# Optimization experiments

Measured on AMD Instinct MI355X. Metric: run time of the kernel, lower is better.

The kernel has to match this reference:

```python
import jax, jax.numpy as jnp
import numpy as np

B, C, W, H = 8, 256, 64, 64
DQK = C // 8  # 32


def setup_inputs() -> dict:
    key = jax.random.key(0)
    ks = jax.random.split(key, 5)
    x = jax.random.normal(ks[0], (B, C, W, H), dtype=jnp.float32)
    # 1x1 conv weights as [out_ch, in_ch]; scaled ~ spectral-normalized magnitude
    w_q = jax.random.normal(ks[1], (DQK, C), dtype=jnp.float32) * (1.0 / np.sqrt(C))
    w_k = jax.random.normal(ks[2], (DQK, C), dtype=jnp.float32) * (1.0 / np.sqrt(C))
    w_v = jax.random.normal(ks[3], (C, C), dtype=jnp.float32) * (1.0 / np.sqrt(C))
    b_q = jnp.zeros((DQK,), dtype=jnp.float32)
    b_k = jnp.zeros((DQK,), dtype=jnp.float32)
    b_v = jnp.zeros((C,), dtype=jnp.float32)
    gamma = jax.random.normal(ks[4], (1,), dtype=jnp.float32)
    return {"x": x, "w_q": w_q, "b_q": b_q, "w_k": w_k, "b_k": b_k,
            "w_v": w_v, "b_v": b_v, "gamma": gamma}


def reference(x, w_q, b_q, w_k, b_k, w_v, b_v, gamma):
    b, c, w, h = x.shape
    n = w * h
    xf = x.reshape(b, c, n)  # [B, C, N]
    # 1x1 convs == channel-mixing matmuls
    q = jnp.einsum('dc,bcn->bnd', w_q, xf) + b_q  # [B, N, Dqk]
    k = jnp.einsum('dc,bcn->bdn', w_k, xf) + b_k[None, :, None]  # [B, Dqk, N]
    v = jnp.einsum('oc,bcn->bon', w_v, xf) + b_v[None, :, None]  # [B, C, N]
    energy = jnp.einsum('bnd,bdm->bnm', q, k)  # [B, N, N]
    attn = jax.nn.softmax(energy, axis=-1)
    # out[b,c,i] = sum_j v[b,c,j] * attn[b,i,j]  (bmm(v, attn^T))
    out = jnp.einsum('bcj,bij->bci', v, attn).reshape(b, c, w, h)
    return gamma[0] * out + x
```

## Files before the change

### kernel.cpp

```cpp
#include <hip/hip_runtime.h>
#include <hip/hip_bf16.h>

typedef __attribute__((ext_vector_type(8))) short short8;
typedef __attribute__((ext_vector_type(4))) float f32x4;
typedef __attribute__((ext_vector_type(16))) float f32x16;

#define NB 8
#define NC 256
#define NN 4096
#define ND 32
#define NCH 16
#define LOG2E 1.44269504088896340736f

#define PIDX(row, col) (((row) << 8) + ((col) ^ (((row) & 15) << 3)))

static __device__ __forceinline__ ushort f2bf(float f) {
  __hip_bfloat16 h = __float2bfloat16(f);
  return reinterpret_cast<ushort&>(h);
}
static __device__ __forceinline__ float bf2f(ushort u) {
  const uint v = ((uint)u) << 16;
  return __builtin_bit_cast(float, v);
}

#define LDW 264
#define LDX 40
#define LDO 136

__global__ __launch_bounds__(256, 2)
void proj_kernel(const float* __restrict__ x,
                 const float* __restrict__ wq, const float* __restrict__ bq,
                 const float* __restrict__ wk, const float* __restrict__ bk,
                 const float* __restrict__ wv, const float* __restrict__ bv,
                 ushort* __restrict__ qk, ushort* __restrict__ vt) {
  __shared__ __align__(16) ushort Ws[2][64 * LDW];
  __shared__ __align__(16) ushort Xs[128 * LDX];

  const int n0 = blockIdx.x * 128;
  const int o0 = blockIdx.y * 64;
  const int b  = blockIdx.z;
  const int t  = threadIdx.x;
  const int w  = t >> 6;
  const int lane = t & 63;
  const int g16  = lane >> 4;
  const int c16  = lane & 15;

  {
    const int o  = t >> 2;
    const int cb = (t & 3) * 64;
    const int oa = o0 + o;
    const float* wrow;
    float scale = 1.0f;
    if (oa < 32)       { wrow = wq + (size_t)oa * NC; scale = LOG2E; }
    else if (oa < 64)  { wrow = wk + (size_t)(oa - 32) * NC; }
    else               { wrow = wv + (size_t)(oa - 64) * NC; }
#pragma unroll
    for (int cc = 0; cc < 64; cc += 8) {
      const float4 f0 = *(const float4*)(wrow + cb + cc);
      const float4 f1 = *(const float4*)(wrow + cb + cc + 4);
      float v[8] = {f0.x, f0.y, f0.z, f0.w, f1.x, f1.y, f1.z, f1.w};
      union { ushort u[8]; uint4 q; } hi, lo;
#pragma unroll
      for (int e = 0; e < 8; ++e) {
        const float s = v[e] * scale;
        const ushort h = f2bf(s);
        hi.u[e] = h;
        lo.u[e] = f2bf(s - bf2f(h));
      }
      *(uint4*)&Ws[0][o * LDW + cb + cc] = hi.q;
      *(uint4*)&Ws[1][o * LDW + cb + cc] = lo.q;
    }
  }

  f32x4 acc[8];
#pragma unroll
  for (int nt = 0; nt < 8; ++nt)
#pragma unroll
    for (int r = 0; r < 4; ++r) acc[nt][r] = 0.f;

  const int s_cc = w * 8 + (lane >> 3);
  const int s_nb = (lane & 7) * 4;

  for (int c0 = 0; c0 < NC; c0 += 32) {
    __syncthreads();
    {
      const float* xsrc = x + ((size_t)(b * NC + c0 + s_cc)) * NN + n0 + s_nb;
#pragma unroll
      for (int it = 0; it < 4; ++it) {
        const float4 f = *(const float4*)(xsrc + it * 32);
        const int n = s_nb + it * 32;
        Xs[(n + 0) * LDX + s_cc] = f2bf(f.x);
        Xs[(n + 1) * LDX + s_cc] = f2bf(f.y);
        Xs[(n + 2) * LDX + s_cc] = f2bf(f.z);
        Xs[(n + 3) * LDX + s_cc] = f2bf(f.w);
      }
    }
    __syncthreads();

    const short8 ah = *(const short8*)&Ws[0][(w * 16 + c16) * LDW + c0 + g16 * 8];
    const short8 al = *(const short8*)&Ws[1][(w * 16 + c16) * LDW + c0 + g16 * 8];
#pragma unroll
    for (int nt = 0; nt < 8; ++nt) {
      const short8 bf = *(const short8*)&Xs[(nt * 16 + c16) * LDX + g16 * 8];
      acc[nt] = __builtin_amdgcn_mfma_f32_16x16x32_bf16(ah, bf, acc[nt], 0, 0, 0);
      acc[nt] = __builtin_amdgcn_mfma_f32_16x16x32_bf16(al, bf, acc[nt], 0, 0, 0);
    }
  }

  if (blockIdx.y == 0) {
    float bb[4];
#pragma unroll
    for (int r = 0; r < 4; ++r) {
      const int o = w * 16 + g16 * 4 + r;
      bb[r] = (o < 32) ? bq[o] * LOG2E : bk[o - 32];
    }
#pragma unroll
    for (int nt = 0; nt < 8; ++nt) {
      union { ushort u[4]; uint2 v; } pk;
#pragma unroll
      for (int r = 0; r < 4; ++r) pk.u[r] = f2bf(acc[nt][r] + bb[r]);
      const int n = n0 + nt * 16 + c16;
      *(uint2*)(qk + ((size_t)(b * NN + n)) * 64 + w * 16 + g16 * 4) = pk.v;
    }
  } else {
    const int ch0 = o0 - 64;
    float bb[4];
#pragma unroll
    for (int r = 0; r < 4; ++r) bb[r] = bv[ch0 + w * 16 + g16 * 4 + r];
    __syncthreads();
    ushort* Os = &Ws[0][0];
#pragma unroll
    for (int nt = 0; nt < 8; ++nt) {
#pragma unroll
      for (int r = 0; r < 4; ++r)
        Os[(w * 16 + g16 * 4 + r) * LDO + nt * 16 + c16] =
            f2bf(acc[nt][r] + bb[r]);
    }
    __syncthreads();
    const int chl = t >> 2;
    const int nb  = (t & 3) * 32;
    ushort* dst = vt + ((size_t)(b * NC + ch0 + chl)) * NN + n0 + nb;
#pragma unroll
    for (int k = 0; k < 4; ++k)
      *(uint4*)(dst + k * 8) = *(const uint4*)&Os[chl * LDO + nb + k * 8];
  }
}

__global__ __launch_bounds__(512, 1)
void attn_kernel(const ushort* __restrict__ qk, const ushort* __restrict__ vt,
                 const float* __restrict__ x, const float* __restrict__ gamma,
                 float* __restrict__ out) {
  __shared__ __align__(16) ushort P[2][128 * 256];
  __shared__ __align__(16) float lL[128];

  const int lin  = blockIdx.x;
  const int b    = lin & 7;
  const int i0   = (lin >> 3) * 128;
  const int t    = threadIdx.x;
  const int w    = t >> 6;
  const int lane = t & 63;
  const int g16  = lane >> 4;
  const int c16  = lane & 15;
  const int l5   = lane >> 5;
  const int c32  = lane & 31;

  const f32x4 zero = {0.f, 0.f, 0.f, 0.f};
  const bool isS = (w < 4);

  const int prow0 = w * 32 + c16;
  const int prow1 = prow0 + 16;
  short8 qf0, qf1;
  short8 kf[8];
  float lp0 = 0.f, lp1 = 0.f;
  const ushort* kbase = qk + ((size_t)b * NN) * 64 + 32 + g16 * 8;
  if (isS) {
    qf0 = *(const short8*)(qk + ((size_t)(b * NN + i0 + prow0)) * 64 + g16 * 8);
    qf1 = *(const short8*)(qk + ((size_t)(b * NN + i0 + prow1)) * 64 + g16 * 8);
  }

  const int p = w - 4;
  f32x16 OA[4], OB[4];
  const ushort* vbA = nullptr; const ushort* vbB = nullptr;
  if (!isS) {
#pragma unroll
    for (int isub = 0; isub < 4; ++isub)
#pragma unroll
      for (int e = 0; e < 16; ++e) { OA[isub][e] = 0.f; OB[isub][e] = 0.f; }
    vbA = vt + ((size_t)(b * NC + p * 64 + c32)) * NN + l5 * 8;
    vbB = vt + ((size_t)(b * NC + p * 64 + 32 + c32)) * NN + l5 * 8;
  }

  for (int iv = 0; iv <= NCH; ++iv) {
    if (isS) {
      if (iv < NCH) {
        ushort* Pb = P[iv & 1];
        const ushort* kch = kbase + (size_t)iv * 256 * 64;
#pragma unroll
        for (int h = 0; h < 2; ++h) {
#pragma unroll
          for (int jt = 0; jt < 8; ++jt)
            kf[jt] = *(const short8*)(
                kch + (size_t)(h * 128 + jt * 16 + c16) * 64);
#pragma unroll
          for (int jt = 0; jt < 8; ++jt) {
            const f32x4 s0 = __builtin_amdgcn_mfma_f32_16x16x32_bf16(
                kf[jt], qf0, zero, 0, 0, 0);
            const f32x4 s1 = __builtin_amdgcn_mfma_f32_16x16x32_bf16(
                kf[jt], qf1, zero, 0, 0, 0);
            union { ushort u[4]; uint2 v; } pk0, pk1;
#pragma unroll
            for (int r = 0; r < 4; ++r) {
              const float e0 = exp2f(s0[r]);
              const float e1 = exp2f(s1[r]);
              lp0 += e0; lp1 += e1;
              pk0.u[r] = f2bf(e0); pk1.u[r] = f2bf(e1);
            }
            const int col = h * 128 + jt * 16 + g16 * 4;
            *(uint2*)&Pb[PIDX(prow0, col)] = pk0.v;
            *(uint2*)&Pb[PIDX(prow1, col)] = pk1.v;
          }
        }
      } else {
        lp0 += __shfl_xor(lp0, 16); lp0 += __shfl_xor(lp0, 32);
        lp1 += __shfl_xor(lp1, 16); lp1 += __shfl_xor(lp1, 32);
        if (g16 == 0) { lL[prow0] = lp0; lL[prow1] = lp1; }
      }
    } else if (iv >= 1) {
      const int ch = iv - 1;
      const ushort* Pb = P[ch & 1];
      const int j0 = ch * 256;
      __builtin_amdgcn_s_setprio(1);
#pragma unroll
      for (int ji = 0; ji < 16; ++ji) {
        const int jo = ji * 16;
        const short8 vf0 = *(const short8*)(vbA + j0 + jo);
        const short8 vf1 = *(const short8*)(vbB + j0 + jo);
#pragma unroll
        for (int isub = 0; isub < 4; ++isub) {
          const short8 pa =
              *(const short8*)&Pb[PIDX(isub * 32 + c32, jo + l5 * 8)];
          OA[isub] = __builtin_amdgcn_mfma_f32_32x32x16_bf16(
              pa, vf0, OA[isub], 0, 0, 0);
          OB[isub] = __builtin_amdgcn_mfma_f32_32x32x16_bf16(
              pa, vf1, OB[isub], 0, 0, 0);
        }
      }
      __builtin_amdgcn_s_setprio(0);
    }
    __syncthreads();
  }

  if (!isS) {
    const float g = gamma[0];
#pragma unroll
    for (int isub = 0; isub < 4; ++isub) {
#pragma unroll
      for (int q = 0; q < 4; ++q) {
        const int r0 = isub * 32 + q * 8 + l5 * 4;
        const f32x4 li = *(const f32x4*)&lL[r0];
        f32x4 gi;
#pragma unroll
        for (int r = 0; r < 4; ++r) gi[r] = g / li[r];
        {
          const int c = p * 64 + c32;
          const size_t base = ((size_t)(b * NC + c)) * NN + i0 + r0;
          const f32x4 xv = *(const f32x4*)(x + base);
          f32x4 ov;
#pragma unroll
          for (int r = 0; r < 4; ++r) ov[r] = OA[isub][q * 4 + r] * gi[r] + xv[r];
          *(f32x4*)(out + base) = ov;
        }
        {
          const int c = p * 64 + 32 + c32;
          const size_t base = ((size_t)(b * NC + c)) * NN + i0 + r0;
          const f32x4 xv = *(const f32x4*)(x + base);
          f32x4 ov;
#pragma unroll
          for (int r = 0; r < 4; ++r) ov[r] = OB[isub][q * 4 + r] * gi[r] + xv[r];
          *(f32x4*)(out + base) = ov;
        }
      }
    }
  }
}

extern "C" void kernel_launch(void* const* d_in, const int* in_sizes, int n_in,
                              void* d_out, int out_size, void* d_ws, size_t ws_size,
                              hipStream_t stream) {
  const float* x  = (const float*)d_in[0];
  const float* wq = (const float*)d_in[1];
  const float* bq = (const float*)d_in[2];
  const float* wk = (const float*)d_in[3];
  const float* bk = (const float*)d_in[4];
  const float* wv = (const float*)d_in[5];
  const float* bv = (const float*)d_in[6];
  const float* gm = (const float*)d_in[7];
  float* outp = (float*)d_out;

  ushort* qkw = (ushort*)d_ws;
  ushort* vtw = qkw + (size_t)NB * NN * 64;

  proj_kernel<<<dim3(NN / 128, 5, NB), 256, 0, stream>>>(
      x, wq, bq, wk, bk, wv, bv, qkw, vtw);
  attn_kernel<<<dim3((NN / 128) * NB), 512, 0, stream>>>(qkw, vtw, x, gm, outp);
}
```

Before: 150.6 us.

## Split PV across eight consumer waves and software-pipeline K and V fragment loads

The attention block grows from 512 to 768 threads, so eight consumer waves each own 32 channels instead of four waves owning 64, which halves the per-wave accumulator registers. Producer waves now double-buffer K fragments across half-chunks, and consumer waves prefetch V fragments two steps ahead in a manually unrolled rotation. The aim is to hide global load latency and raise MFMA throughput per block. In exchange, the 3-blocks-per-SM launch bound tightens the register budget and the 128KB shared P buffer likely still limits occupancy to one block.

```diff
diff --git a/kernel.cpp b/kernel.cpp
--- a/kernel.cpp
+++ b/kernel.cpp
@@ -146,7 +146,47 @@
   }
 }
 
-__global__ __launch_bounds__(512, 1)
+#define S_JT(KF, COL)                                                         \
+  do {                                                                        \
+    const f32x4 s0 = __builtin_amdgcn_mfma_f32_16x16x32_bf16(KF, qf0, zero,   \
+                                                             0, 0, 0);        \
+    const f32x4 s1 = __builtin_amdgcn_mfma_f32_16x16x32_bf16(KF, qf1, zero,   \
+                                                             0, 0, 0);        \
+    union { ushort u[4]; uint2 v; } pk0, pk1;                                 \
+    _Pragma("unroll")                                                         \
+    for (int r = 0; r < 4; ++r) {                                             \
+      const float e0 = exp2f(s0[r]);                                          \
+      const float e1 = exp2f(s1[r]);                                          \
+      lp0 += e0; lp1 += e1;                                                   \
+      pk0.u[r] = f2bf(e0); pk1.u[r] = f2bf(e1);                               \
+    }                                                                         \
+    *(uint2*)&Pb[PIDX(prow0, (COL) + g16 * 4)] = pk0.v;                       \
+    *(uint2*)&Pb[PIDX(prow1, (COL) + g16 * 4)] = pk1.v;                       \
+  } while (0)
+
+#define KLOAD(KF, J0)                                                         \
+  do {                                                                        \
+    _Pragma("unroll")                                                         \
+    for (int jt = 0; jt < 8; ++jt)                                            \
+      KF[jt] = *(const short8*)(kbase + (size_t)((J0) + jt * 16 + c16) * 64); \
+  } while (0)
+
+#define PVL(JI) (*(const short8*)(vptr + j0 + (JI) * 16))
+
+#define PVC(VF, JI)                                                           \
+  do {                                                                        \
+    const int jo = (JI) * 16;                                                 \
+    const short8 pa0 = *(const short8*)&Pb[PIDX(0 * 32 + c32, jo + l5 * 8)];  \
+    const short8 pa1 = *(const short8*)&Pb[PIDX(1 * 32 + c32, jo + l5 * 8)];  \
+    const short8 pa2 = *(const short8*)&Pb[PIDX(2 * 32 + c32, jo + l5 * 8)];  \
+    const short8 pa3 = *(const short8*)&Pb[PIDX(3 * 32 + c32, jo + l5 * 8)];  \
+    OA[0] = __builtin_amdgcn_mfma_f32_32x32x16_bf16(pa0, VF, OA[0], 0, 0, 0); \
+    OA[1] = __builtin_amdgcn_mfma_f32_32x32x16_bf16(pa1, VF, OA[1], 0, 0, 0); \
+    OA[2] = __builtin_amdgcn_mfma_f32_32x32x16_bf16(pa2, VF, OA[2], 0, 0, 0); \
+    OA[3] = __builtin_amdgcn_mfma_f32_32x32x16_bf16(pa3, VF, OA[3], 0, 0, 0); \
+  } while (0)
+
+__global__ __launch_bounds__(768, 3)
 void attn_kernel(const ushort* __restrict__ qk, const ushort* __restrict__ vt,
                  const float* __restrict__ x, const float* __restrict__ gamma,
                  float* __restrict__ out) {
@@ -170,56 +210,39 @@
   const int prow0 = w * 32 + c16;
   const int prow1 = prow0 + 16;
   short8 qf0, qf1;
-  short8 kf[8];
+  short8 kfA[8], kfB[8];
   float lp0 = 0.f, lp1 = 0.f;
   const ushort* kbase = qk + ((size_t)b * NN) * 64 + 32 + g16 * 8;
   if (isS) {
     qf0 = *(const short8*)(qk + ((size_t)(b * NN + i0 + prow0)) * 64 + g16 * 8);
     qf1 = *(const short8*)(qk + ((size_t)(b * NN + i0 + prow1)) * 64 + g16 * 8);
+    KLOAD(kfA, 0);
   }
 
   const int p = w - 4;
-  f32x16 OA[4], OB[4];
-  const ushort* vbA = nullptr; const ushort* vbB = nullptr;
+  f32x16 OA[4];
+  const ushort* vptr = nullptr;
   if (!isS) {
 #pragma unroll
     for (int isub = 0; isub < 4; ++isub)
 #pragma unroll
-      for (int e = 0; e < 16; ++e) { OA[isub][e] = 0.f; OB[isub][e] = 0.f; }
-    vbA = vt + ((size_t)(b * NC + p * 64 + c32)) * NN + l5 * 8;
-    vbB = vt + ((size_t)(b * NC + p * 64 + 32 + c32)) * NN + l5 * 8;
+      for (int e = 0; e < 16; ++e) OA[isub][e] = 0.f;
+    vptr = vt + ((size_t)(b * NC + p * 32 + c32)) * NN + l5 * 8;
   }
 
   for (int iv = 0; iv <= NCH; ++iv) {
     if (isS) {
       if (iv < NCH) {
         ushort* Pb = P[iv & 1];
-        const ushort* kch = kbase + (size_t)iv * 256 * 64;
-#pragma unroll
-        for (int h = 0; h < 2; ++h) {
-#pragma unroll
-          for (int jt = 0; jt < 8; ++jt)
-            kf[jt] = *(const short8*)(
-                kch + (size_t)(h * 128 + jt * 16 + c16) * 64);
-#pragma unroll
-          for (int jt = 0; jt < 8; ++jt) {
-            const f32x4 s0 = __builtin_amdgcn_mfma_f32_16x16x32_bf16(
-                kf[jt], qf0, zero, 0, 0, 0);
-            const f32x4 s1 = __builtin_amdgcn_mfma_f32_16x16x32_bf16(
-                kf[jt], qf1, zero, 0, 0, 0);
-            union { ushort u[4]; uint2 v; } pk0, pk1;
-#pragma unroll
-            for (int r = 0; r < 4; ++r) {
-              const float e0 = exp2f(s0[r]);
-              const float e1 = exp2f(s1[r]);
-              lp0 += e0; lp1 += e1;
-              pk0.u[r] = f2bf(e0); pk1.u[r] = f2bf(e1);
-            }
-            const int col = h * 128 + jt * 16 + g16 * 4;
-            *(uint2*)&Pb[PIDX(prow0, col)] = pk0.v;
-            *(uint2*)&Pb[PIDX(prow1, col)] = pk1.v;
-          }
-        }
+        const int j0 = iv * 256;
+        KLOAD(kfB, j0 + 128);
+        S_JT(kfA[0], 0);   S_JT(kfA[1], 16);  S_JT(kfA[2], 32);
+        S_JT(kfA[3], 48);  S_JT(kfA[4], 64);  S_JT(kfA[5], 80);
+        S_JT(kfA[6], 96);  S_JT(kfA[7], 112);
+        if (iv + 1 < NCH) KLOAD(kfA, j0 + 256);
+        S_JT(kfB[0], 128); S_JT(kfB[1], 144); S_JT(kfB[2], 160);
+        S_JT(kfB[3], 176); S_JT(kfB[4], 192); S_JT(kfB[5], 208);
+        S_JT(kfB[6], 224); S_JT(kfB[7], 240);
       } else {
         lp0 += __shfl_xor(lp0, 16); lp0 += __shfl_xor(lp0, 32);
         lp1 += __shfl_xor(lp1, 16); lp1 += __shfl_xor(lp1, 32);
@@ -229,22 +252,24 @@
       const int ch = iv - 1;
       const ushort* Pb = P[ch & 1];
       const int j0 = ch * 256;
+      short8 v_a, v_b, v_c;
+      v_a = PVL(0);  v_b = PVL(1);
       __builtin_amdgcn_s_setprio(1);
-#pragma unroll
-      for (int ji = 0; ji < 16; ++ji) {
-        const int jo = ji * 16;
-        const short8 vf0 = *(const short8*)(vbA + j0 + jo);
-        const short8 vf1 = *(const short8*)(vbB + j0 + jo);
-#pragma unroll
-        for (int isub = 0; isub < 4; ++isub) {
-          const short8 pa =
-              *(const short8*)&Pb[PIDX(isub * 32 + c32, jo + l5 * 8)];
-          OA[isub] = __builtin_amdgcn_mfma_f32_32x32x16_bf16(
-              pa, vf0, OA[isub], 0, 0, 0);
-          OB[isub] = __builtin_amdgcn_mfma_f32_32x32x16_bf16(
-              pa, vf1, OB[isub], 0, 0, 0);
-        }
-      }
+      v_c = PVL(2);   PVC(v_a, 0);
+      v_a = PVL(3);   PVC(v_b, 1);
+      v_b = PVL(4);   PVC(v_c, 2);
+      v_c = PVL(5);   PVC(v_a, 3);
+      v_a = PVL(6);   PVC(v_b, 4);
+      v_b = PVL(7);   PVC(v_c, 5);
+      v_c = PVL(8);   PVC(v_a, 6);
+      v_a = PVL(9);   PVC(v_b, 7);
+      v_b = PVL(10);  PVC(v_c, 8);
+      v_c = PVL(11);  PVC(v_a, 9);
+      v_a = PVL(12);  PVC(v_b, 10);
+      v_b = PVL(13);  PVC(v_c, 11);
+      v_c = PVL(14);  PVC(v_a, 12);
+      v_a = PVL(15);  PVC(v_b, 13);
+      PVC(v_c, 14);   PVC(v_a, 15);
       __builtin_amdgcn_s_setprio(0);
     }
     __syncthreads();
@@ -261,24 +286,13 @@
         f32x4 gi;
 #pragma unroll
         for (int r = 0; r < 4; ++r) gi[r] = g / li[r];
-        {
-          const int c = p * 64 + c32;
-          const size_t base = ((size_t)(b * NC + c)) * NN + i0 + r0;
-          const f32x4 xv = *(const f32x4*)(x + base);
-          f32x4 ov;
-#pragma unroll
-          for (int r = 0; r < 4; ++r) ov[r] = OA[isub][q * 4 + r] * gi[r] + xv[r];
-          *(f32x4*)(out + base) = ov;
-        }
-        {
-          const int c = p * 64 + 32 + c32;
-          const size_t base = ((size_t)(b * NC + c)) * NN + i0 + r0;
-          const f32x4 xv = *(const f32x4*)(x + base);
-          f32x4 ov;
-#pragma unroll
-          for (int r = 0; r < 4; ++r) ov[r] = OB[isub][q * 4 + r] * gi[r] + xv[r];
-          *(f32x4*)(out + base) = ov;
-        }
+        const int c = p * 32 + c32;
+        const size_t base = ((size_t)(b * NC + c)) * NN + i0 + r0;
+        const f32x4 xv = *(const f32x4*)(x + base);
+        f32x4 ov;
+#pragma unroll
+        for (int r = 0; r < 4; ++r) ov[r] = OA[isub][q * 4 + r] * gi[r] + xv[r];
+        *(f32x4*)(out + base) = ov;
       }
     }
   }
@@ -302,5 +316,5 @@
 
   proj_kernel<<<dim3(NN / 128, 5, NB), 256, 0, stream>>>(
       x, wq, bq, wk, bk, wv, bv, qkw, vtw);
-  attn_kernel<<<dim3((NN / 128) * NB), 512, 0, stream>>>(qkw, vtw, x, gm, outp);
-}
+  attn_kernel<<<dim3((NN / 128) * NB), 768, 0, stream>>>(qkw, vtw, x, gm, outp);
+}
```

Result: slower. 307.6 us (+104.3%).

## Split PV accumulation across eight consumer waves and prefetch V fragments

Applied to the files above, without the earlier changes.

Grows the attention block from 512 to 768 threads, so eight consumer waves each accumulate 32 output channels instead of four waves handling 64. This halves the per-wave accumulator state and MFMA chain and adds waves that can hide latency while producer waves compute P. It also double-buffers the V fragment loads in registers, so the next load is issued before the current MFMAs run. The cost is that every consumer wave still reads the full P tile, which doubles LDS read traffic for P. The launch bounds change also alters register budgeting and could cause spills.

```diff
diff --git a/kernel.cpp b/kernel.cpp
--- a/kernel.cpp
+++ b/kernel.cpp
@@ -146,7 +146,7 @@
   }
 }
 
-__global__ __launch_bounds__(512, 1)
+__global__ __launch_bounds__(768, 3)
 void attn_kernel(const ushort* __restrict__ qk, const ushort* __restrict__ vt,
                  const float* __restrict__ x, const float* __restrict__ gamma,
                  float* __restrict__ out) {
@@ -179,15 +179,14 @@
   }
 
   const int p = w - 4;
-  f32x16 OA[4], OB[4];
-  const ushort* vbA = nullptr; const ushort* vbB = nullptr;
+  f32x16 OA[4];
+  const ushort* vptr = nullptr;
   if (!isS) {
 #pragma unroll
     for (int isub = 0; isub < 4; ++isub)
 #pragma unroll
-      for (int e = 0; e < 16; ++e) { OA[isub][e] = 0.f; OB[isub][e] = 0.f; }
-    vbA = vt + ((size_t)(b * NC + p * 64 + c32)) * NN + l5 * 8;
-    vbB = vt + ((size_t)(b * NC + p * 64 + 32 + c32)) * NN + l5 * 8;
+      for (int e = 0; e < 16; ++e) OA[isub][e] = 0.f;
+    vptr = vt + ((size_t)(b * NC + p * 32 + c32)) * NN + l5 * 8;
   }
 
   for (int iv = 0; iv <= NCH; ++iv) {
@@ -229,20 +228,21 @@
       const int ch = iv - 1;
       const ushort* Pb = P[ch & 1];
       const int j0 = ch * 256;
+      short8 vf[2];
+      vf[0] = *(const short8*)(vptr + j0);
       __builtin_amdgcn_s_setprio(1);
 #pragma unroll
       for (int ji = 0; ji < 16; ++ji) {
+        if (ji + 1 < 16)
+          vf[(ji + 1) & 1] = *(const short8*)(vptr + j0 + (ji + 1) * 16);
         const int jo = ji * 16;
-        const short8 vf0 = *(const short8*)(vbA + j0 + jo);
-        const short8 vf1 = *(const short8*)(vbB + j0 + jo);
+        const short8 v0 = vf[ji & 1];
 #pragma unroll
         for (int isub = 0; isub < 4; ++isub) {
           const short8 pa =
               *(const short8*)&Pb[PIDX(isub * 32 + c32, jo + l5 * 8)];
           OA[isub] = __builtin_amdgcn_mfma_f32_32x32x16_bf16(
-              pa, vf0, OA[isub], 0, 0, 0);
-          OB[isub] = __builtin_amdgcn_mfma_f32_32x32x16_bf16(
-              pa, vf1, OB[isub], 0, 0, 0);
+              pa, v0, OA[isub], 0, 0, 0);
         }
       }
       __builtin_amdgcn_s_setprio(0);
@@ -261,24 +261,13 @@
         f32x4 gi;
 #pragma unroll
         for (int r = 0; r < 4; ++r) gi[r] = g / li[r];
-        {
-          const int c = p * 64 + c32;
-          const size_t base = ((size_t)(b * NC + c)) * NN + i0 + r0;
-          const f32x4 xv = *(const f32x4*)(x + base);
-          f32x4 ov;
-#pragma unroll
-          for (int r = 0; r < 4; ++r) ov[r] = OA[isub][q * 4 + r] * gi[r] + xv[r];
-          *(f32x4*)(out + base) = ov;
-        }
-        {
-          const int c = p * 64 + 32 + c32;
-          const size_t base = ((size_t)(b * NC + c)) * NN + i0 + r0;
-          const f32x4 xv = *(const f32x4*)(x + base);
-          f32x4 ov;
-#pragma unroll
-          for (int r = 0; r < 4; ++r) ov[r] = OB[isub][q * 4 + r] * gi[r] + xv[r];
-          *(f32x4*)(out + base) = ov;
-        }
+        const int c = p * 32 + c32;
+        const size_t base = ((size_t)(b * NC + c)) * NN + i0 + r0;
+        const f32x4 xv = *(const f32x4*)(x + base);
+        f32x4 ov;
+#pragma unroll
+        for (int r = 0; r < 4; ++r) ov[r] = OA[isub][q * 4 + r] * gi[r] + xv[r];
+        *(f32x4*)(out + base) = ov;
       }
     }
   }
@@ -302,5 +291,5 @@
 
   proj_kernel<<<dim3(NN / 128, 5, NB), 256, 0, stream>>>(
       x, wq, bq, wk, bk, wv, bv, qkw, vtw);
-  attn_kernel<<<dim3((NN / 128) * NB), 512, 0, stream>>>(qkw, vtw, x, gm, outp);
-}
+  attn_kernel<<<dim3((NN / 128) * NB), 768, 0, stream>>>(qkw, vtw, x, gm, outp);
+}
```

Result: no change. 151.7 us (+0.7%).
